# Kernel optimization log

Measured on AMD Instinct MI355X. Metric: run time of the kernel, lower is better.

## Reference

```python
import jax, jax.numpy as jnp
import numpy as np

B, T = 4, 2048
IN_DIM = 128          # eff_in_dim == eff_out_dim (n_groups = 1)
IN_POINTS = 32
OUT_POINTS = 32
QUERY_DIM = 256
OUT_QUERY_DIM = 256
HIDDEN = QUERY_DIM // 4                       # 64
CHANNEL_PARAMS = IN_DIM * IN_DIM              # 16384
SPATIAL_PARAMS = OUT_POINTS * IN_POINTS       # 1024
TOTAL_PARAMS = CHANNEL_PARAMS + SPATIAL_PARAMS  # 17408
LN_EPS = 1e-6


def setup_inputs() -> dict:
    key = jax.random.key(0)
    ks = jax.random.split(key, 10)
    inp = {
        "sampled": jax.random.normal(ks[0], (B, T, 1, IN_POINTS, IN_DIM), jnp.float32),
        "query": jax.random.normal(ks[1], (B, T, QUERY_DIM), jnp.float32),
        # parameter_generator: LayerNorm(QUERY_DIM) -> Linear(QUERY_DIM, HIDDEN) -> Linear(HIDDEN, TOTAL_PARAMS)
        "ln_w": jnp.ones((QUERY_DIM,), jnp.float32) * QUERY_DIM ** -0.5,
        "ln_b": jnp.zeros((QUERY_DIM,), jnp.float32),
        "w1": jax.random.normal(ks[2], (HIDDEN, QUERY_DIM), jnp.float32) * 0.05,
        "b1": jax.random.normal(ks[3], (HIDDEN,), jnp.float32) * 0.02,
        "w2": jax.random.normal(ks[4], (TOTAL_PARAMS, HIDDEN), jnp.float32) * 0.05,
        "b2": jax.random.normal(ks[5], (TOTAL_PARAMS,), jnp.float32) * 0.05,
        "m_beta": jnp.zeros((IN_DIM,), jnp.float32),
        "s_beta": jnp.zeros((OUT_POINTS,), jnp.float32),
        "wo": jax.random.normal(ks[6], (OUT_QUERY_DIM, IN_DIM * OUT_POINTS), jnp.float32) * 0.02,
        "bo": jax.random.normal(ks[7], (OUT_QUERY_DIM,), jnp.float32) * 0.02,
    }
    return inp


def reference(sampled, query, ln_w, ln_b, w1, b1, w2, b2, m_beta, s_beta, wo, bo):
    b, t, g, P, C = sampled.shape  # g == 1
    BT = b * t
    OP = s_beta.shape[0]

    # parameter generator: LN -> Linear -> Linear (no activation in between)
    mu = jnp.mean(query, axis=-1, keepdims=True)
    var = jnp.var(query, axis=-1, keepdims=True)
    q = (query - mu) * jax.lax.rsqrt(var + LN_EPS) * ln_w + ln_b
    h = q @ w1.T + b1                               # [B, T, HIDDEN]
    params = (h @ w2.T + b2).reshape(BT, -1)        # [BT, TOTAL_PARAMS]

    channel_mixing = params[:, : C * C].reshape(BT, C, C)      # [BT, C, C]
    spatial_mixing = params[:, C * C :].reshape(BT, OP, P)     # [BT, OP, P]

    x = sampled.reshape(BT, P, C)
    # channel mixing: baddbmm(m_beta, x, channel_mixing) then GELU (exact/erf)
    x = jax.nn.gelu(jnp.einsum("bpc,bcd->bpd", x, channel_mixing) + m_beta,
                    approximate=False)
    # spatial mixing: baddbmm(s_beta, spatial_mixing, x) then GELU
    x = jax.nn.gelu(jnp.einsum("bop,bpd->bod", spatial_mixing, x) + s_beta[:, None],
                    approximate=False)

    out = x.reshape(b, t, -1) @ wo.T + bo           # [B, T, OUT_QUERY_DIM]
    return out
```

## Files before the change

### kernel.cpp

```cpp
#include <hip/hip_runtime.h>
#include <cstdint>


typedef __bf16 bf16x8 __attribute__((ext_vector_type(8)));
typedef float  f32x4  __attribute__((ext_vector_type(4)));
typedef unsigned short ushort;
typedef ushort ushort8 __attribute__((ext_vector_type(8)));

#define TW 16

__device__ __forceinline__ ushort f2b(float f) {
    union { float f; uint32_t u; } v; v.f = f;
    uint32_t u = v.u;
    u += 0x7fffu + ((u >> 16) & 1u);
    return (ushort)(u >> 16);
}
__device__ __forceinline__ uint32_t pk2(float a, float b) {
    return (uint32_t)f2b(a) | ((uint32_t)f2b(b) << 16);
}
__device__ __forceinline__ float gelu_fast(float x) {
    float z = fabsf(x) * 0.70710678118654752440f;
    float t = __builtin_amdgcn_rcpf(fmaf(0.3275911f, z, 1.0f));
    float p = t * fmaf(t, fmaf(t, fmaf(t, fmaf(t, 1.061405429f, -1.453152027f),
                                       1.421413741f), -0.284496736f), 0.254829592f);
    float e = __expf(-z * z);
    float erfv = copysignf(fmaf(-p, e, 1.0f), x);
    return 0.5f * x * (1.0f + erfv);
}

__global__ void prep(const float* __restrict__ w2, const float* __restrict__ w1,
                     const float* __restrict__ wo, const float* __restrict__ b2,
                     ushort* __restrict__ w2p, ushort* __restrict__ w2sp,
                     ushort* __restrict__ w1p, ushort* __restrict__ wop,
                     float* __restrict__ b2t) {
    int i = blockIdx.x * 256 + threadIdx.x;
    {
        int j = i & 7, l = (i >> 3) & 63, ks = (i >> 9) & 1;
        int d = (i >> 10) & 127, cb = (i >> 17) & 7;
        w2p[i] = f2b(w2[(size_t)((cb * 16 + (l & 15)) * 128 + d) * 64 +
                        ks * 32 + (l >> 4) * 8 + j]);
    }
    {
        int j = i & 7, l = (i >> 3) & 63, nb = (i >> 9) & 15, kc5 = (i >> 13) & 127;
        int o = (l >> 4) * 8 + j, q = nb * 16 + (l & 15);
        int d16 = kc5 & 15, dt2 = kc5 >> 4;
        wop[i] = f2b(wo[(size_t)q * 4096 + o * 128 + dt2 * 16 + d16]);
    }
    if (i < 65536) {
        int j = i & 7, l = (i >> 3) & 63, ks = (i >> 9) & 1, g = (i >> 10) & 63;
        w2sp[i] = f2b(w2[(size_t)(16384 + g * 16 + (l & 15)) * 64 +
                         ks * 32 + (l >> 4) * 8 + j]);
    }
    if (i < 16384) {
        int j = i & 7, l = (i >> 3) & 63, ks = (i >> 9) & 7, nb = i >> 12;
        w1p[i] = f2b(w1[(nb * 16 + (l & 15)) * 256 + ks * 32 + (l >> 4) * 8 + j]);
        b2t[i] = b2[(i & 127) * 128 + (i >> 7)];
    }
}

__launch_bounds__(512, 2)
__global__ void fused(const float* __restrict__ sampled, const float* __restrict__ query,
                      const float* __restrict__ ln_w, const float* __restrict__ ln_b,
                      const float* __restrict__ b1, const float* __restrict__ b2,
                      const float* __restrict__ m_beta, const float* __restrict__ s_beta,
                      const ushort* __restrict__ w2p, const ushort* __restrict__ w2sp,
                      const ushort* __restrict__ w1p, const float* __restrict__ b2t,
                      ushort* __restrict__ y2f) {
    __shared__ ushort Hb[TW * 64];
    __shared__ union {
        ushort qn[TW * 264];
        ushort smT[TW * 1032];
        struct {
            ushort pt[TW * 1032];
            ushort g1s[TW * 640];
        } mp;
    } U;
    __shared__ float mb_s[128];
    __shared__ float sb_s[32];

    const int tid  = threadIdx.x;
    const int wv   = tid >> 6;
    const int lane = tid & 63;
    const int lq   = lane >> 4;
    const int ln16 = lane & 15;
    const int tok0 = blockIdx.x * TW;

    if (tid < 128) mb_s[tid] = m_beta[tid];
    else if (tid < 160) sb_s[tid - 128] = s_beta[tid - 128];

    for (int tt = 0; tt < 2; ++tt) {
        int t = wv * 2 + tt;
        const float* q = query + (size_t)(tok0 + t) * 256;
        float2 a = *(const float2*)(q + 2 * lane);
        float2 b = *(const float2*)(q + 128 + 2 * lane);
        float s = a.x + a.y + b.x + b.y;
        for (int off = 1; off < 64; off <<= 1) s += __shfl_xor(s, off);
        float mu = s * (1.0f / 256.0f);
        float d0 = a.x - mu, d1 = a.y - mu, d2 = b.x - mu, d3 = b.y - mu;
        float ss = d0 * d0 + d1 * d1 + d2 * d2 + d3 * d3;
        for (int off = 1; off < 64; off <<= 1) ss += __shfl_xor(ss, off);
        float rstd = rsqrtf(ss * (1.0f / 256.0f) + 1e-6f);
        int i0 = 2 * lane, i1 = 2 * lane + 128;
        float q0 = d0 * rstd * ln_w[i0]     + ln_b[i0];
        float q1 = d1 * rstd * ln_w[i0 + 1] + ln_b[i0 + 1];
        float q2 = d2 * rstd * ln_w[i1]     + ln_b[i1];
        float q3 = d3 * rstd * ln_w[i1 + 1] + ln_b[i1 + 1];
        *(uint32_t*)&U.qn[t * 264 + i0] = pk2(q0, q1);
        *(uint32_t*)&U.qn[t * 264 + i1] = pk2(q2, q3);
    }
    __syncthreads();

    if (wv < 4) {
        int nb = wv;
        f32x4 acc = {0.0f, 0.0f, 0.0f, 0.0f};
        for (int ks = 0; ks < 8; ++ks) {
            bf16x8 afr = *(const bf16x8*)&U.qn[ln16 * 264 + ks * 32 + lq * 8];
            bf16x8 bfr = *(const bf16x8*)&w1p[(nb * 8 + ks) * 512 + lane * 8];
            acc = __builtin_amdgcn_mfma_f32_16x16x32_bf16(afr, bfr, acc, 0, 0, 0);
        }
        float bias = b1[nb * 16 + ln16];
        for (int i = 0; i < 4; ++i) {
            int t = lq * 4 + i;
            Hb[t * 64 + nb * 16 + ln16] = f2b(acc[i] + bias);
        }
    }
    __syncthreads();

    bf16x8 hfr[2];
    hfr[0] = *(const bf16x8*)&Hb[ln16 * 64 + 0 + lq * 8];
    hfr[1] = *(const bf16x8*)&Hb[ln16 * 64 + 32 + lq * 8];

    for (int gi = 0; gi < 8; ++gi) {
        int g = wv * 8 + gi;
        f32x4 acc = *(const f32x4*)&b2[16384 + g * 16 + lq * 4];
        for (int ks = 0; ks < 2; ++ks) {
            bf16x8 afr = *(const bf16x8*)&w2sp[(g * 2 + ks) * 512 + lane * 8];
            acc = __builtin_amdgcn_mfma_f32_16x16x32_bf16(afr, hfr[ks], acc, 0, 0, 0);
        }
        int o = g >> 1;
        int p0 = (g & 1) * 16 + lq * 4;
        uint2 wr;
        wr.x = pk2(acc[0], acc[1]);
        wr.y = pk2(acc[2], acc[3]);
        *(uint2*)&U.smT[ln16 * 1032 + o * 32 + p0] = wr;
    }

    bf16x8 xa[2][2][4];
    for (int tt = 0; tt < 2; ++tt) {
        const float* xp = sampled + (size_t)(tok0 + wv * 2 + tt) * 4096;
        for (int mt = 0; mt < 2; ++mt) {
            int p = mt * 16 + ln16;
            for (int ks = 0; ks < 4; ++ks) {
                int c = ks * 32 + lq * 8;
                float4 lo = *(const float4*)(xp + p * 128 + c);
                float4 hi = *(const float4*)(xp + p * 128 + c + 4);
                ushort8 u;
                u[0] = f2b(lo.x); u[1] = f2b(lo.y); u[2] = f2b(lo.z); u[3] = f2b(lo.w);
                u[4] = f2b(hi.x); u[5] = f2b(hi.y); u[6] = f2b(hi.z); u[7] = f2b(hi.w);
                xa[tt][mt][ks] = __builtin_bit_cast(bf16x8, u);
            }
        }
    }
    __syncthreads();

    bf16x8 sa[2][2];
    for (int tt = 0; tt < 2; ++tt) {
        int t = wv * 2 + tt;
        for (int mt = 0; mt < 2; ++mt)
            sa[tt][mt] = *(const bf16x8*)&U.smT[t * 1032 + (mt * 16 + ln16) * 32 + lq * 8];
    }
    __syncthreads();

    for (int dt = 0; dt < 16; ++dt) {
        const int cb = wv;
        for (int dd = 0; dd < 8; ++dd) {
            int d = dt * 8 + dd;
            f32x4 acc = *(const f32x4*)&b2t[d * 128 + cb * 16 + lq * 4];
            for (int ks = 0; ks < 2; ++ks) {
                bf16x8 afr = *(const bf16x8*)&w2p[((cb * 128 + d) * 2 + ks) * 512 + lane * 8];
                acc = __builtin_amdgcn_mfma_f32_16x16x32_bf16(afr, hfr[ks], acc, 0, 0, 0);
            }
            uint2 wr;
            wr.x = pk2(acc[0], acc[1]);
            wr.y = pk2(acc[2], acc[3]);
            *(uint2*)&U.mp.pt[ln16 * 1032 + ((cb * 2 + (lq >> 1)) * 8 + dd) * 8 + (lq & 1) * 4] = wr;
        }
        __syncthreads();

        const int ddl = ln16 & 7;
        const bool hi = ln16 >= 8;
        for (int tt = 0; tt < 2; ++tt) {
            int t = wv * 2 + tt;
            bf16x8 bfr[4];
            for (int ks = 0; ks < 4; ++ks)
                bfr[ks] = *(const bf16x8*)&U.mp.pt[t * 1032 + (ks * 4 + lq) * 64 + ddl * 8];
            float mb = mb_s[dt * 8 + ddl];
            for (int mt = 0; mt < 2; ++mt) {
                f32x4 acc = {0.0f, 0.0f, 0.0f, 0.0f};
                for (int ks = 0; ks < 4; ++ks)
                    acc = __builtin_amdgcn_mfma_f32_16x16x32_bf16(xa[tt][mt][ks], bfr[ks], acc, 0, 0, 0);
                float va = hi ? acc[2] : acc[0];
                float vb = hi ? acc[3] : acc[1];
                float ga = gelu_fast(va + mb);
                float gb = gelu_fast(vb + mb);
                int p = mt * 16 + lq * 4 + (hi ? 2 : 0);
                *(uint32_t*)&U.mp.g1s[t * 640 + ((dt & 1) * 8 + ddl) * 40 + p] = pk2(ga, gb);
            }
        }

        if (dt & 1) {
            __builtin_amdgcn_wave_barrier();
            int dt2 = dt >> 1;
            for (int tt = 0; tt < 2; ++tt) {
                int t = wv * 2 + tt;
                bf16x8 gb = *(const bf16x8*)&U.mp.g1s[t * 640 + ln16 * 40 + lq * 8];
                for (int mt = 0; mt < 2; ++mt) {
                    f32x4 acc = {0.0f, 0.0f, 0.0f, 0.0f};
                    acc = __builtin_amdgcn_mfma_f32_16x16x32_bf16(sa[tt][mt], gb, acc, 0, 0, 0);
                    float4 sbv = *(const float4*)&sb_s[mt * 16 + lq * 4];
                    float g0 = gelu_fast(acc[0] + sbv.x);
                    float g1 = gelu_fast(acc[1] + sbv.y);
                    float g2 = gelu_fast(acc[2] + sbv.z);
                    float g3 = gelu_fast(acc[3] + sbv.w);
                    uint2 wr;
                    wr.x = pk2(g0, g1);
                    wr.y = pk2(g2, g3);
                    size_t addr = (size_t)blockIdx.x * 65536 +
                                  (dt2 * 16 + ln16) * 512 +
                                  (t + (mt * 2 + (lq >> 1)) * 16) * 8 + (lq & 1) * 4;
                    *(uint2*)&y2f[addr] = wr;
                }
            }
        }
        __syncthreads();
    }
}

__launch_bounds__(512, 2)
__global__ void outproj(const ushort* __restrict__ y2f, const ushort* __restrict__ wop,
                        const float* __restrict__ bo, float* __restrict__ out) {
    const int tid  = threadIdx.x;
    const int wv   = tid >> 6;
    const int lane = tid & 63;
    const int lq   = lane >> 4;
    const int ln16 = lane & 15;
    const int tb   = blockIdx.x;

    f32x4 acc[2][2];
    for (int m = 0; m < 2; ++m)
        for (int n = 0; n < 2; ++n) acc[m][n] = (f32x4){0.0f, 0.0f, 0.0f, 0.0f};

    const ushort* a0 = y2f + (size_t)(tb * 2) * 65536 + lane * 8;
    const ushort* a1 = a0 + 65536;
    const ushort* bp = wop + (size_t)(wv * 2) * 512 + lane * 8;

    #pragma unroll 4
    for (int k = 0; k < 128; ++k) {
        bf16x8 af0 = *(const bf16x8*)(a0 + k * 512);
        bf16x8 af1 = *(const bf16x8*)(a1 + k * 512);
        bf16x8 bf0 = *(const bf16x8*)(bp + (size_t)k * 8192);
        bf16x8 bf1 = *(const bf16x8*)(bp + (size_t)k * 8192 + 512);
        acc[0][0] = __builtin_amdgcn_mfma_f32_16x16x32_bf16(af0, bf0, acc[0][0], 0, 0, 0);
        acc[0][1] = __builtin_amdgcn_mfma_f32_16x16x32_bf16(af0, bf1, acc[0][1], 0, 0, 0);
        acc[1][0] = __builtin_amdgcn_mfma_f32_16x16x32_bf16(af1, bf0, acc[1][0], 0, 0, 0);
        acc[1][1] = __builtin_amdgcn_mfma_f32_16x16x32_bf16(af1, bf1, acc[1][1], 0, 0, 0);
    }

    for (int n = 0; n < 2; ++n) {
        int q = (wv * 2 + n) * 16 + ln16;
        float bov = bo[q];
        for (int m = 0; m < 2; ++m)
            for (int i = 0; i < 4; ++i) {
                int tok = tb * 32 + m * 16 + lq * 4 + i;
                out[(size_t)tok * 256 + q] = acc[m][n][i] + bov;
            }
    }
}

extern "C" void kernel_launch(void* const* d_in, const int* in_sizes, int n_in,
                              void* d_out, int out_size, void* d_ws, size_t ws_size,
                              hipStream_t stream) {
    const float* sampled = (const float*)d_in[0];
    const float* query   = (const float*)d_in[1];
    const float* ln_w    = (const float*)d_in[2];
    const float* ln_b    = (const float*)d_in[3];
    const float* w1      = (const float*)d_in[4];
    const float* b1      = (const float*)d_in[5];
    const float* w2      = (const float*)d_in[6];
    const float* b2      = (const float*)d_in[7];
    const float* m_beta  = (const float*)d_in[8];
    const float* s_beta  = (const float*)d_in[9];
    const float* wo      = (const float*)d_in[10];
    const float* bo      = (const float*)d_in[11];
    float* out = (float*)d_out;

    char* ws = (char*)d_ws;
    ushort* w2p  = (ushort*)(ws);
    ushort* wop  = (ushort*)(ws + 2097152);
    ushort* w2sp = (ushort*)(ws + 4194304);
    ushort* w1p  = (ushort*)(ws + 4325376);
    float*  b2t  = (float*) (ws + 4358144);
    ushort* y2f  = (ushort*)(ws + 4423680);

    prep<<<4096, 256, 0, stream>>>(w2, w1, wo, b2, w2p, w2sp, w1p, wop, b2t);
    fused<<<512, 512, 0, stream>>>(sampled, query, ln_w, ln_b, b1, b2,
                                   m_beta, s_beta, w2p, w2sp, w1p, b2t, y2f);
    outproj<<<256, 512, 0, stream>>>(y2f, wop, bo, out);
}
```

Before: 391.4 us.

## Fuse output projection into main kernel via shared-memory staging and deferred accumulation

Removes the separate outproj kernel and the bf16 y2f round trip through global memory. Spatial-mixing GELU outputs now go into a shared-memory tile, and each half-chunk is folded into output-projection accumulators one iteration later, overlapping with the next channel-mixing step. This saves a kernel launch and the intermediate write and read. In exchange each 16-token block re-reads the full wo weights, so weight traffic is higher than with the 32-token tiles of the old outproj, and shared memory and register use grow.

```diff
diff --git a/kernel.cpp b/kernel.cpp
--- a/kernel.cpp
+++ b/kernel.cpp
@@ -65,7 +65,8 @@
                       const float* __restrict__ m_beta, const float* __restrict__ s_beta,
                       const ushort* __restrict__ w2p, const ushort* __restrict__ w2sp,
                       const ushort* __restrict__ w1p, const float* __restrict__ b2t,
-                      ushort* __restrict__ y2f) {
+                      const ushort* __restrict__ wop, const float* __restrict__ bo,
+                      float* __restrict__ out) {
     __shared__ ushort Hb[TW * 64];
     __shared__ union {
         ushort qn[TW * 264];
@@ -75,6 +76,7 @@
             ushort g1s[TW * 640];
         } mp;
     } U;
+    __shared__ __align__(16) ushort g2t[TW * 16 * 32];
     __shared__ float mb_s[128];
     __shared__ float sb_s[32];
 
@@ -171,7 +173,23 @@
     }
     __syncthreads();
 
+    f32x4 aco[2] = {(f32x4){0.0f, 0.0f, 0.0f, 0.0f}, (f32x4){0.0f, 0.0f, 0.0f, 0.0f}};
+
+    auto outacc = [&](int dt2) {
+        const ushort* wb = wop + ((size_t)(dt2 * 16) * 16 + wv * 2) * 512 + lane * 8;
+        const char* gpb = (const char*)g2t + ln16 * 1024 + lq * 16;
+        for (int d16 = 0; d16 < 16; ++d16) {
+            bf16x8 afr = *(const bf16x8*)(gpb + d16 * 64);
+            bf16x8 bf0 = *(const bf16x8*)(wb + (size_t)d16 * 8192);
+            bf16x8 bf1 = *(const bf16x8*)(wb + (size_t)d16 * 8192 + 512);
+            aco[0] = __builtin_amdgcn_mfma_f32_16x16x32_bf16(afr, bf0, aco[0], 0, 0, 0);
+            aco[1] = __builtin_amdgcn_mfma_f32_16x16x32_bf16(afr, bf1, aco[1], 0, 0, 0);
+        }
+    };
+
     for (int dt = 0; dt < 16; ++dt) {
+        if (dt && !(dt & 1)) outacc((dt >> 1) - 1);
+
         const int cb = wv;
         for (int dd = 0; dd < 8; ++dd) {
             int d = dt * 8 + dd;
@@ -210,13 +228,12 @@
 
         if (dt & 1) {
             __builtin_amdgcn_wave_barrier();
-            int dt2 = dt >> 1;
             for (int tt = 0; tt < 2; ++tt) {
                 int t = wv * 2 + tt;
-                bf16x8 gb = *(const bf16x8*)&U.mp.g1s[t * 640 + ln16 * 40 + lq * 8];
+                bf16x8 gfr = *(const bf16x8*)&U.mp.g1s[t * 640 + ln16 * 40 + lq * 8];
                 for (int mt = 0; mt < 2; ++mt) {
                     f32x4 acc = {0.0f, 0.0f, 0.0f, 0.0f};
-                    acc = __builtin_amdgcn_mfma_f32_16x16x32_bf16(sa[tt][mt], gb, acc, 0, 0, 0);
+                    acc = __builtin_amdgcn_mfma_f32_16x16x32_bf16(sa[tt][mt], gfr, acc, 0, 0, 0);
                     float4 sbv = *(const float4*)&sb_s[mt * 16 + lq * 4];
                     float g0 = gelu_fast(acc[0] + sbv.x);
                     float g1 = gelu_fast(acc[1] + sbv.y);
@@ -225,55 +242,21 @@
                     uint2 wr;
                     wr.x = pk2(g0, g1);
                     wr.y = pk2(g2, g3);
-                    size_t addr = (size_t)blockIdx.x * 65536 +
-                                  (dt2 * 16 + ln16) * 512 +
-                                  (t + (mt * 2 + (lq >> 1)) * 16) * 8 + (lq & 1) * 4;
-                    *(uint2*)&y2f[addr] = wr;
+                    *(uint2*)((char*)g2t + t * 1024 + ln16 * 64 + mt * 32 + lq * 8) = wr;
                 }
             }
         }
         __syncthreads();
     }
-}
-
-__launch_bounds__(512, 2)
-__global__ void outproj(const ushort* __restrict__ y2f, const ushort* __restrict__ wop,
-                        const float* __restrict__ bo, float* __restrict__ out) {
-    const int tid  = threadIdx.x;
-    const int wv   = tid >> 6;
-    const int lane = tid & 63;
-    const int lq   = lane >> 4;
-    const int ln16 = lane & 15;
-    const int tb   = blockIdx.x;
-
-    f32x4 acc[2][2];
-    for (int m = 0; m < 2; ++m)
-        for (int n = 0; n < 2; ++n) acc[m][n] = (f32x4){0.0f, 0.0f, 0.0f, 0.0f};
-
-    const ushort* a0 = y2f + (size_t)(tb * 2) * 65536 + lane * 8;
-    const ushort* a1 = a0 + 65536;
-    const ushort* bp = wop + (size_t)(wv * 2) * 512 + lane * 8;
-
-    #pragma unroll 4
-    for (int k = 0; k < 128; ++k) {
-        bf16x8 af0 = *(const bf16x8*)(a0 + k * 512);
-        bf16x8 af1 = *(const bf16x8*)(a1 + k * 512);
-        bf16x8 bf0 = *(const bf16x8*)(bp + (size_t)k * 8192);
-        bf16x8 bf1 = *(const bf16x8*)(bp + (size_t)k * 8192 + 512);
-        acc[0][0] = __builtin_amdgcn_mfma_f32_16x16x32_bf16(af0, bf0, acc[0][0], 0, 0, 0);
-        acc[0][1] = __builtin_amdgcn_mfma_f32_16x16x32_bf16(af0, bf1, acc[0][1], 0, 0, 0);
-        acc[1][0] = __builtin_amdgcn_mfma_f32_16x16x32_bf16(af1, bf0, acc[1][0], 0, 0, 0);
-        acc[1][1] = __builtin_amdgcn_mfma_f32_16x16x32_bf16(af1, bf1, acc[1][1], 0, 0, 0);
-    }
-
+
+    outacc(7);
     for (int n = 0; n < 2; ++n) {
         int q = (wv * 2 + n) * 16 + ln16;
-        float bov = bo[q];
-        for (int m = 0; m < 2; ++m)
-            for (int i = 0; i < 4; ++i) {
-                int tok = tb * 32 + m * 16 + lq * 4 + i;
-                out[(size_t)tok * 256 + q] = acc[m][n][i] + bov;
-            }
+        float bv = bo[q];
+        for (int i = 0; i < 4; ++i) {
+            int tok = tok0 + lq * 4 + i;
+            out[(size_t)tok * 256 + q] = aco[n][i] + bv;
+        }
     }
 }
 
@@ -300,10 +283,9 @@
     ushort* w2sp = (ushort*)(ws + 4194304);
     ushort* w1p  = (ushort*)(ws + 4325376);
     float*  b2t  = (float*) (ws + 4358144);
-    ushort* y2f  = (ushort*)(ws + 4423680);
 
     prep<<<4096, 256, 0, stream>>>(w2, w1, wo, b2, w2p, w2sp, w1p, wop, b2t);
     fused<<<512, 512, 0, stream>>>(sampled, query, ln_w, ln_b, b1, b2,
-                                   m_beta, s_beta, w2p, w2sp, w1p, b2t, y2f);
-    outproj<<<256, 512, 0, stream>>>(y2f, wop, bo, out);
-}
+                                   m_beta, s_beta, w2p, w2sp, w1p, b2t,
+                                   wop, bo, out);
+}
```

Measured after the change: 392.8 us. No clear change (+0.3%).
